# Kernel optimization log

Measured on AMD Instinct MI355X. Metric: run time of the kernel, lower is better.

## Reference

```python
import jax, jax.numpy as jnp
import numpy as np
from jax import lax

IMG_W, IMG_H = 800.0, 320.0
NPTS = 72
N_STRIPS = NPTS - 1
MAX_LANES = 4
NUM_PRIORS = 192
STAGES = 3
B = 512
LIOU_LEN = 15.0
CLS_W, XYT_W, IOU_W, SEG_W = 2.0, 0.2, 2.0, 1.0


def smooth_l1(x):
    ax = jnp.abs(x)
    return jnp.where(ax < 1.0, 0.5 * x * x, ax - 0.5)


def pairwise_line_iou(pred_xs, tgt_xs):
    # pred_xs [P,N] pixel xs, tgt_xs [L,N]; returns [P,L]
    px1, px2 = pred_xs - LIOU_LEN, pred_xs + LIOU_LEN
    tx1, tx2 = tgt_xs - LIOU_LEN, tgt_xs + LIOU_LEN
    ovr = jnp.minimum(px2[:, None, :], tx2[None]) - jnp.maximum(px1[:, None, :], tx1[None])
    union = jnp.maximum(px2[:, None, :], tx2[None]) - jnp.minimum(px1[:, None, :], tx1[None])
    invalid = (tgt_xs < 0) | (tgt_xs >= IMG_W)
    ovr = jnp.where(invalid[None], 0.0, ovr)
    union = jnp.where(invalid[None], 0.0, union)
    return ovr.sum(-1) / (union.sum(-1) + 1e-9)


def focal_sum(logits, target):
    # kornia-style softmax focal loss (alpha=0.25, gamma=2), summed
    p = jax.nn.softmax(logits, axis=1) + 1e-8
    focal = -0.25 * (1.0 - p) ** 2 * jnp.log(p)
    oh = jax.nn.one_hot(target, 2, dtype=logits.dtype)
    return (oh * focal).sum()


def per_sample(pred, tgt):
    # pred [P, 6+N], tgt [L, 6+N]
    L = tgt.shape[0]
    f32 = pred.dtype
    valid = tgt[:, 1] == 1.0
    num_t = valid.sum()
    has_t = num_t > 0

    t_xs = tgt[:, 6:]                          # [L,N] pixel xs (-1e5 = invalid)
    pred_xs_px = pred[:, 6:] * (IMG_W - 1.0)   # [P,N]
    iou_pair = pairwise_line_iou(pred_xs_px, t_xs)  # [P,L] (grad flows for loss)

    # ---------- assignment (stop-grad, mirrors CLRNet dynamic_assign) ----------
    pd = lax.stop_gradient(pred)
    pd_xs = pd[:, 6:] * (IMG_W - 1.0)
    inv_t = (t_xs < 0) | (t_xs >= IMG_W)
    t_len = (~inv_t).sum(1).astype(f32)
    dist = jnp.where(inv_t[None], 0.0, jnp.abs(t_xs[None] - pd_xs[:, None, :])).sum(-1)
    dist = dist / (t_len[None] + 1e-9)         # [P,L]

    def norm_score(x):
        m = jnp.max(jnp.where(valid[None], x, -jnp.inf))
        m = jnp.where(has_t, m, 1.0)
        return 1.0 - x / m + 1e-2

    dist_score = norm_score(dist)
    p_xy = jnp.stack([pd[:, 2] * (IMG_H - 1.0), pd[:, 3] * (IMG_W - 1.0)], 1)
    t_xy = jnp.stack([tgt[:, 2] * (IMG_H - 1.0), tgt[:, 3]], 1)
    sd = jnp.sqrt(((p_xy[:, None] - t_xy[None]) ** 2).sum(-1))
    s_score = norm_score(sd)
    th = jnp.abs(pd[:, 4, None] - tgt[None, :, 4]) * 180.0
    th_score = norm_score(th)
    sp = jax.nn.sigmoid(pd[:, :2])
    neg = -jnp.log(1.0 - sp + 1e-12) * 0.75 * sp ** 2
    pos = -jnp.log(sp + 1e-12) * 0.25 * (1.0 - sp) ** 2
    cls_cost = pos[:, 1] - neg[:, 1]           # all gt labels are 1
    cost = -(dist_score * s_score * th_score) ** 2 * 3.0 + cls_cost[:, None]
    cost = jnp.where(valid[None], cost, jnp.inf)

    # dynamic-k (SimOTA-style)
    iou_sg = jnp.where(valid[None], jnp.maximum(lax.stop_gradient(iou_pair), 0.0), 0.0)
    topk = lax.top_k(iou_sg.T, 4)[0]           # [L,4]
    dyn_k = jnp.maximum(topk.sum(1).astype(jnp.int32), 1)
    ranks = jnp.argsort(jnp.argsort(cost, axis=0), axis=0)
    M = (ranks < dyn_k[None]) & valid[None]
    multi = M.sum(1) > 1
    argmin_col = jnp.argmin(cost, axis=1)
    Mf = M.astype(f32)
    Mf = Mf.at[:, 0].set(jnp.where(multi, 0.0, Mf[:, 0]))
    oh_min = jax.nn.one_hot(argmin_col, L, dtype=f32)
    Mf = jnp.where(multi[:, None] & (oh_min > 0), 1.0, Mf)
    n_match = Mf.sum()

    # ---------- cls loss ----------
    cls_target = (Mf.sum(1) > 0).astype(jnp.int32)
    cls_term = focal_sum(pred[:, :2], cls_target) / jnp.where(has_t, num_t.astype(f32), 1.0)

    # ---------- reg yxtl (smooth L1) ----------
    scale = jnp.array([N_STRIPS, IMG_W - 1.0, 180.0, N_STRIPS], dtype=f32)
    pred_yxtl = pred[:, 2:6] * scale           # [P,4]
    tgt3 = jnp.stack([tgt[:, 2] * N_STRIPS, tgt[:, 3], tgt[:, 4] * 180.0], 1)  # [L,3]
    pred_starts = jnp.clip(jnp.round(lax.stop_gradient(pred[:, 2]) * N_STRIPS), 0, N_STRIPS)
    tgt_starts = jnp.round(tgt[:, 2] * N_STRIPS)
    tgt_len_pair = tgt[None, :, 5] - (pred_starts[:, None] - tgt_starts[None, :])  # [P,L]
    sl = smooth_l1(pred_yxtl[:, None, :3] - tgt3[None]).sum(-1) \
       + smooth_l1(pred_yxtl[:, 3][:, None] - tgt_len_pair)
    reg_term = (Mf * sl).sum() / jnp.maximum(n_match * 4.0, 1.0)
    iou_term = (Mf * (1.0 - iou_pair)).sum() / jnp.maximum(n_match, 1.0)
    zero = jnp.zeros((), f32)
    reg_term = jnp.where(has_t, reg_term, zero)
    iou_term = jnp.where(has_t, iou_term, zero)
    return cls_term, reg_term, iou_term


def setup_inputs() -> dict:
    key = jax.random.key(0)
    ks = jax.random.split(key, 8)
    D = 6 + NPTS
    cls = jax.random.normal(ks[0], (STAGES, B, NUM_PRIORS, 2), jnp.float32)
    rest = jax.random.uniform(ks[1], (STAGES, B, NUM_PRIORS, D - 2), dtype=jnp.float32)
    predictions = jnp.concatenate([cls, rest], -1)

    valid = jax.random.uniform(ks[2], (B, MAX_LANES)) < 0.8
    start = jax.random.randint(ks[3], (B, MAX_LANES), 0, 40)
    length = jax.random.randint(ks[4], (B, MAX_LANES), 10, NPTS)
    end = jnp.minimum(start + length, NPTS)
    idx = jnp.arange(NPTS)
    inside = (idx[None, None] >= start[..., None]) & (idx[None, None] < end[..., None]) & valid[..., None]
    xs = jax.random.uniform(ks[5], (B, MAX_LANES, NPTS), minval=0.0, maxval=IMG_W - 1.0)
    xs = jnp.where(inside, xs, -1e5)
    start_x = jnp.take_along_axis(xs, start[..., None], axis=-1)[..., 0]
    theta = jax.random.uniform(ks[6], (B, MAX_LANES), minval=0.3, maxval=0.9)
    vf = valid.astype(jnp.float32)
    neg = jnp.full((B, MAX_LANES), -1e5, jnp.float32)
    targets = jnp.full((B, MAX_LANES, D), -1e5, jnp.float32)
    targets = targets.at[..., 0].set(1.0 - vf)
    targets = targets.at[..., 1].set(vf)
    targets = targets.at[..., 2].set(jnp.where(valid, start.astype(jnp.float32) / N_STRIPS, neg))
    targets = targets.at[..., 3].set(jnp.where(valid, start_x, neg))
    targets = targets.at[..., 4].set(jnp.where(valid, theta, neg))
    targets = targets.at[..., 5].set(jnp.where(valid, (end - start).astype(jnp.float32), neg))
    targets = targets.at[..., 6:].set(xs)

    seg_loss = jax.random.uniform(ks[7], (), dtype=jnp.float32)
    return {"predictions": predictions, "targets": targets, "seg_loss": seg_loss}


def reference(predictions, targets, seg_loss):
    per_batch = jax.vmap(per_sample)
    cls_l = jnp.zeros((), predictions.dtype)
    reg_l = jnp.zeros((), predictions.dtype)
    iou_l = jnp.zeros((), predictions.dtype)
    for s in range(predictions.shape[0]):  # 3 refine stages (fixed)
        c, r, i = per_batch(predictions[s], targets)
        cls_l = cls_l + c.sum()
        reg_l = reg_l + r.sum()
        iou_l = iou_l + i.sum()
    denom = targets.shape[0] * predictions.shape[0]
    cls_l = cls_l / denom
    reg_l = reg_l / denom
    iou_l = iou_l / denom
    return cls_l * CLS_W + reg_l * XYT_W + iou_l * IOU_W + seg_loss * SEG_W
```

## Files before the change

kernel.cpp:

```cpp
#include <hip/hip_runtime.h>
#include <math.h>

constexpr int kNpts   = 72;
constexpr int kPriors = 192;
constexpr int kLanes  = 4;
constexpr int kBatch  = 512;
constexpr int kStages = 3;
constexpr int kD      = 6 + kNpts;
constexpr int kBlocks = kStages * kBatch;

typedef unsigned long long u64;

__device__ __forceinline__ float smoothL1(float x) {
  float ax = fabsf(x);
  return ax < 1.0f ? 0.5f * x * x : ax - 0.5f;
}

__device__ __forceinline__ unsigned ordF(float f) {
  unsigned b = __float_as_uint(f);
  return (b & 0x80000000u) ? ~b : (b | 0x80000000u);
}

__device__ __forceinline__ void cswapA(u64& a, u64& b) {
  if (b < a) { u64 t = a; a = b; b = t; }
}
__device__ __forceinline__ void cswapD(float& a, float& b) {
  if (b > a) { float t = a; a = b; b = t; }
}
__device__ __forceinline__ u64 umin64(u64 a, u64 b) { return a < b ? a : b; }
__device__ __forceinline__ u64 umax64(u64 a, u64 b) { return a < b ? b : a; }

#define STEP(K, PV) {                                         \
    const float4 t_ = tx4[(K)];                               \
    const float p_ = (PV) * 799.0f;                           \
    ds0 += (t_.x >= 0.0f) ? fabsf(t_.x - p_) : 0.0f;          \
    ds1 += (t_.y >= 0.0f) ? fabsf(t_.y - p_) : 0.0f;          \
    ds2 += (t_.z >= 0.0f) ? fabsf(t_.z - p_) : 0.0f;          \
    ds3 += (t_.w >= 0.0f) ? fabsf(t_.w - p_) : 0.0f; }

#define BATCH18(K0, B)                                            \
    STEP((K0) + 0,  (B##0).x) STEP((K0) + 1,  (B##0).y)           \
    STEP((K0) + 2,  (B##1).x) STEP((K0) + 3,  (B##1).y)           \
    STEP((K0) + 4,  (B##2).x) STEP((K0) + 5,  (B##2).y)           \
    STEP((K0) + 6,  (B##3).x) STEP((K0) + 7,  (B##3).y)           \
    STEP((K0) + 8,  (B##4).x) STEP((K0) + 9,  (B##4).y)           \
    STEP((K0) + 10, (B##5).x) STEP((K0) + 11, (B##5).y)           \
    STEP((K0) + 12, (B##6).x) STEP((K0) + 13, (B##6).y)           \
    STEP((K0) + 14, (B##7).x) STEP((K0) + 15, (B##7).y)           \
    STEP((K0) + 16, (B##8).x) STEP((K0) + 17, (B##8).y)

#define LOADB(B, I0)                                          \
    B##0 = rowv[(I0) + 0]; B##1 = rowv[(I0) + 1];             \
    B##2 = rowv[(I0) + 2]; B##3 = rowv[(I0) + 3];             \
    B##4 = rowv[(I0) + 4]; B##5 = rowv[(I0) + 5];             \
    B##6 = rowv[(I0) + 6]; B##7 = rowv[(I0) + 7];             \
    B##8 = rowv[(I0) + 8];

__global__ __launch_bounds__(192) void clr_loss_kernel(
    const float* __restrict__ pred,
    const float* __restrict__ tgt,
    float* __restrict__ partial) {
  const int blk  = blockIdx.x;
  const int b    = blk & (kBatch - 1);
  const int tid  = threadIdx.x;
  const int wav  = tid >> 6;
  const int lane = tid & 63;

  __shared__ __align__(16) float s_tx[kNpts][kLanes];
  __shared__ float s_hdr[kLanes][6];
  __shared__ float s_cost[kLanes][kPriors];
  __shared__ float s_iou[kLanes][kPriors];
  __shared__ u64   s_k3[kLanes][3];
  __shared__ int   s_dk[kLanes];
  __shared__ float s_sc[3][4];

  const float* tg = tgt + (size_t)b * kLanes * kD;
  for (int t = tid; t < kLanes * kNpts; t += 192) {
    int j = t / kNpts, k = t - j * kNpts;
    s_tx[k][j] = tg[j * kD + 6 + k];
  }
  if (tid < kLanes * 6) {
    int j = tid / 6, c = tid - j * 6;
    s_hdr[j][c] = tg[j * kD + c];
  }
  if (tid >= 64 && tid < 64 + kLanes) {
    int j = tid - 64;
    s_dk[j] = 1; s_k3[j][0] = 0; s_k3[j][1] = 0; s_k3[j][2] = 0;
  }

  const float*  pr   = pred + ((size_t)blk * kPriors + tid) * kD;
  const float2* rowv = (const float2*)pr;
  float2 h0 = rowv[0], h1 = rowv[1], h2 = rowv[2];
  float2 a0, a1, a2, a3, a4, a5, a6, a7, a8;
  float2 b0, b1, b2, b3, b4, b5, b6, b7, b8;
  LOADB(a, 3)
  LOADB(b, 12)
  const float p0 = h0.x, p1 = h0.y, p2 = h1.x, p3 = h1.y, p4 = h2.x, p5 = h2.y;

  __syncthreads();

  bool validL[kLanes];
  int num_t = 0;
#pragma unroll
  for (int j = 0; j < kLanes; ++j) {
    validL[j] = (s_hdr[j][1] == 1.0f);
    num_t += validL[j] ? 1 : 0;
  }
  const bool has_t = num_t > 0;

  float ds0 = 0.0f, ds1 = 0.0f, ds2 = 0.0f, ds3 = 0.0f;
  {
    const float4* tx4 = (const float4*)&s_tx[0][0];
    BATCH18(0, a)
    LOADB(a, 21)
    BATCH18(18, b)
    LOADB(b, 30)
    BATCH18(36, a)
    BATCH18(54, b)
  }
  float ds[kLanes] = {ds0, ds1, ds2, ds3};

  float iou[kLanes], dist[kLanes], sd[kLanes], th[kLanes];
  float md = -INFINITY, ms = -INFINITY, mt = -INFINITY;
  const float py = p2 * 319.0f, pxc = p3 * 799.0f;
#pragma unroll
  for (int j = 0; j < kLanes; ++j) {
    float tlen = validL[j] ? s_hdr[j][5] : 0.0f;
    float ovr = fmaf(tlen, 30.0f, -ds[j]);
    float uni = fmaf(tlen, 30.0f,  ds[j]) + 1e-9f;
    iou[j]  = ovr / uni;
    dist[j] = ds[j] / (tlen + 1e-9f);
    float dy = py - s_hdr[j][2] * 319.0f;
    float dx = pxc - s_hdr[j][3];
    sd[j] = sqrtf(dy * dy + dx * dx);
    th[j] = fabsf(p4 - s_hdr[j][4]) * 180.0f;
    if (validL[j]) {
      md = fmaxf(md, dist[j]);
      ms = fmaxf(ms, sd[j]);
      mt = fmaxf(mt, th[j]);
    }
  }

#pragma unroll
  for (int off = 32; off; off >>= 1) {
    md = fmaxf(md, __shfl_down(md, off, 64));
    ms = fmaxf(ms, __shfl_down(ms, off, 64));
    mt = fmaxf(mt, __shfl_down(mt, off, 64));
  }
  if (lane == 0) { s_sc[wav][0] = md; s_sc[wav][1] = ms; s_sc[wav][2] = mt; }
  __syncthreads();
  md = fmaxf(fmaxf(s_sc[0][0], s_sc[1][0]), s_sc[2][0]);
  ms = fmaxf(fmaxf(s_sc[0][1], s_sc[1][1]), s_sc[2][1]);
  mt = fmaxf(fmaxf(s_sc[0][2], s_sc[1][2]), s_sc[2][2]);
  if (!has_t) { md = 1.0f; ms = 1.0f; mt = 1.0f; }

  const float sp1  = 1.0f / (1.0f + expf(-p1));
  const float neg1 = -logf(1.0f - sp1 + 1e-12f) * 0.75f * sp1 * sp1;
  const float om1  = 1.0f - sp1;
  const float pos1 = -logf(sp1 + 1e-12f) * 0.25f * om1 * om1;
  const float cls_cost = pos1 - neg1;

  float costr[kLanes];
#pragma unroll
  for (int j = 0; j < kLanes; ++j) {
    s_iou[j][tid] = validL[j] ? fmaxf(iou[j], 0.0f) : 0.0f;
    float c;
    if (validL[j]) {
      float a = (1.0f - dist[j] / md) + 0.01f;
      float s = (1.0f - sd[j] / ms) + 0.01f;
      float t = (1.0f - th[j] / mt) + 0.01f;
      float g = a * s * t;
      c = cls_cost - g * g * 3.0f;
    } else {
      c = INFINITY;
    }
    costr[j] = c;
    s_cost[j][tid] = c;
  }
  __syncthreads();

  for (int t = wav; t < 8; t += 3) {
    const int j = t & 3;
    if (!validL[j]) continue;
    if (t < 4) {
      float c0 = s_cost[j][lane], c1 = s_cost[j][lane + 64], c2 = s_cost[j][lane + 128];
      u64 k0 = ((u64)ordF(c0) << 32) | (unsigned)lane;
      u64 k1 = ((u64)ordF(c1) << 32) | (unsigned)(lane + 64);
      u64 k2 = ((u64)ordF(c2) << 32) | (unsigned)(lane + 128);
      cswapA(k0, k1); cswapA(k0, k2); cswapA(k1, k2);
#pragma unroll
      for (int off = 1; off < 64; off <<= 1) {
        u64 b0 = __shfl_xor(k0, off), b1 = __shfl_xor(k1, off), b2 = __shfl_xor(k2, off);
        u64 x0 = umin64(k0, b0), y0 = umax64(k0, b0);
        u64 x1 = umin64(k1, b1);
        u64 mc = umin64(k2, b2);
        k0 = x0;
        k2 = umin64(umax64(y0, x1), mc);
        k1 = umin64(y0, x1);
      }
      if (lane == 0) { s_k3[j][0] = k0; s_k3[j][1] = k1; s_k3[j][2] = k2; }
    } else {
      float t0 = s_iou[j][lane], t1 = s_iou[j][lane + 64], t2 = s_iou[j][lane + 128];
      float t3 = -1.0f;
      cswapD(t0, t1); cswapD(t0, t2); cswapD(t1, t2);
#pragma unroll
      for (int off = 1; off < 64; off <<= 1) {
        float b0 = __shfl_xor(t0, off), b1 = __shfl_xor(t1, off);
        float b2 = __shfl_xor(t2, off), b3 = __shfl_xor(t3, off);
        float m0 = fmaxf(t0, b3), m1 = fmaxf(t1, b2);
        float m2 = fmaxf(t2, b1), m3 = fmaxf(t3, b0);
        cswapD(m0, m2); cswapD(m1, m3); cswapD(m0, m1); cswapD(m2, m3);
        t0 = m0; t1 = m1; t2 = m2; t3 = m3;
      }
      if (lane == 0) {
        float s = ((t0 + t1) + t2) + t3;
        int dk = (int)s;
        if (dk < 1) dk = 1;
        if (dk > 3) dk = 3;
        s_dk[j] = dk;
      }
    }
  }
  __syncthreads();

  int Mi[kLanes];
  int msum = 0;
#pragma unroll
  for (int j = 0; j < kLanes; ++j) {
    u64 myk = ((u64)ordF(costr[j]) << 32) | (unsigned)tid;
    Mi[j] = (validL[j] && myk <= s_k3[j][s_dk[j] - 1]) ? 1 : 0;
    msum += Mi[j];
  }

  float amin = costr[0];
  int aidx = 0;
#pragma unroll
  for (int j = 1; j < kLanes; ++j)
    if (costr[j] < amin) { amin = costr[j]; aidx = j; }

  float Mf[kLanes];
#pragma unroll
  for (int j = 0; j < kLanes; ++j) Mf[j] = (float)Mi[j];
  if (msum > 1) {
    Mf[0] = 0.0f;
    Mf[aidx] = 1.0f;
  }

  const float mfsum = Mf[0] + Mf[1] + Mf[2] + Mf[3];
  const int cls_t = (mfsum > 0.0f) ? 1 : 0;

  const float mx = fmaxf(p0, p1);
  const float e0 = expf(p0 - mx), e1 = expf(p1 - mx);
  const float inv = 1.0f / (e0 + e1);
  const float q = (cls_t ? e1 : e0) * inv + 1e-8f;
  const float omq = 1.0f - q;
  const float focal = -0.25f * omq * omq * logf(q);

  const float pred_start = fminf(fmaxf(rintf(p2 * 71.0f), 0.0f), 71.0f);
  const float py0 = p2 * 71.0f, py1 = p3 * 799.0f, py2t = p4 * 180.0f, py3 = p5 * 71.0f;
  float regc = 0.0f, iouc = 0.0f;
#pragma unroll
  for (int j = 0; j < kLanes; ++j) {
    if (Mf[j] > 0.0f) {
      float t30 = s_hdr[j][2] * 71.0f;
      float t31 = s_hdr[j][3];
      float t32 = s_hdr[j][4] * 180.0f;
      float tstart = rintf(s_hdr[j][2] * 71.0f);
      float tlp = s_hdr[j][5] - (pred_start - tstart);
      regc += smoothL1(py0 - t30) + smoothL1(py1 - t31) + smoothL1(py2t - t32)
            + smoothL1(py3 - tlp);
      iouc += 1.0f - iou[j];
    }
  }

  float v0 = mfsum, v1 = focal, v2 = regc, v3 = iouc;
#pragma unroll
  for (int off = 32; off; off >>= 1) {
    v0 += __shfl_down(v0, off, 64);
    v1 += __shfl_down(v1, off, 64);
    v2 += __shfl_down(v2, off, 64);
    v3 += __shfl_down(v3, off, 64);
  }
  __syncthreads();
  if (lane == 0) {
    s_sc[wav][0] = v0; s_sc[wav][1] = v1; s_sc[wav][2] = v2; s_sc[wav][3] = v3;
  }
  __syncthreads();

  if (tid == 0) {
    float nm      = s_sc[0][0] + s_sc[1][0] + s_sc[2][0];
    float cls_sum = s_sc[0][1] + s_sc[1][1] + s_sc[2][1];
    float reg_sum = s_sc[0][2] + s_sc[1][2] + s_sc[2][2];
    float iou_sum = s_sc[0][3] + s_sc[1][3] + s_sc[2][3];

    float cls_term = cls_sum / (has_t ? (float)num_t : 1.0f);
    float reg_term = has_t ? reg_sum / fmaxf(nm * 4.0f, 1.0f) : 0.0f;
    float iou_term = has_t ? iou_sum / fmaxf(nm, 1.0f) : 0.0f;

    partial[blk] = 2.0f * cls_term + 0.2f * reg_term + 2.0f * iou_term;
  }
}

#undef STEP
#undef BATCH18
#undef LOADB

__global__ __launch_bounds__(256) void clr_reduce(
    const float* __restrict__ partial,
    const float* __restrict__ seg,
    float* __restrict__ out) {
  const int tid  = threadIdx.x;
  const int wav  = tid >> 6;
  const int lane = tid & 63;
  __shared__ float sc[4];

  float s = 0.0f;
#pragma unroll
  for (int i = 0; i < kBlocks / 256; ++i) s += partial[tid + 256 * i];
#pragma unroll
  for (int off = 32; off; off >>= 1) s += __shfl_down(s, off, 64);
  if (lane == 0) sc[wav] = s;
  __syncthreads();
  if (tid == 0) {
    float tot = ((sc[0] + sc[1]) + sc[2]) + sc[3];
    out[0] = tot * (1.0f / (float)kBlocks) + seg[0];
  }
}

extern "C" void kernel_launch(void* const* d_in, const int* in_sizes, int n_in,
                              void* d_out, int out_size, void* d_ws, size_t ws_size,
                              hipStream_t stream) {
  const float* pred = (const float*)d_in[0];
  const float* tgt  = (const float*)d_in[1];
  const float* seg  = (const float*)d_in[2];
  float* out     = (float*)d_out;
  float* partial = (float*)d_ws;

  clr_loss_kernel<<<kBlocks, 192, 0, stream>>>(pred, tgt, partial);
  clr_reduce<<<1, 256, 0, stream>>>(partial, seg, out);
}
```

Measured before the change: 149.0 us.

## Stage prediction tile into LDS with coalesced global_load_lds DMA

Before this change, each thread loaded its own 312-byte prediction row straight from global memory with strided float2 loads. Now the block's whole 192x78 prediction tile is copied into shared memory with 16-byte global_load_lds transfers, where each wave copies contiguous 1 KB chunks, so the global reads are fully coalesced. The per-row distance loop then reads from LDS in a simple unrolled loop instead of juggling two register batches. The cost is about 60 KB of extra LDS per block, which lowers blocks per CU. Row-strided LDS reads may also hit bank conflicts, and the register-level prefetch overlap is lost.

```diff
diff --git a/kernel.cpp b/kernel.cpp
--- a/kernel.cpp
+++ b/kernel.cpp
@@ -8,6 +8,9 @@
 constexpr int kStages = 3;
 constexpr int kD      = 6 + kNpts;
 constexpr int kBlocks = kStages * kBatch;
+constexpr int kTileF  = kPriors * kD;
+constexpr int kTileB  = kTileF * 4;
+constexpr int kChunks = kTileB / 1024;
 
 typedef unsigned long long u64;
 
@@ -29,6 +32,12 @@
 }
 __device__ __forceinline__ u64 umin64(u64 a, u64 b) { return a < b ? a : b; }
 __device__ __forceinline__ u64 umax64(u64 a, u64 b) { return a < b ? b : a; }
+
+__device__ __forceinline__ void gload_lds16(const void* g, void* l) {
+  __builtin_amdgcn_global_load_lds(
+      (const __attribute__((address_space(1))) void*)g,
+      (__attribute__((address_space(3))) void*)l, 16, 0, 0);
+}
 
 #define STEP(K, PV) {                                         \
     const float4 t_ = tx4[(K)];                               \
@@ -37,24 +46,6 @@
     ds1 += (t_.y >= 0.0f) ? fabsf(t_.y - p_) : 0.0f;          \
     ds2 += (t_.z >= 0.0f) ? fabsf(t_.z - p_) : 0.0f;          \
     ds3 += (t_.w >= 0.0f) ? fabsf(t_.w - p_) : 0.0f; }
-
-#define BATCH18(K0, B)                                            \
-    STEP((K0) + 0,  (B##0).x) STEP((K0) + 1,  (B##0).y)           \
-    STEP((K0) + 2,  (B##1).x) STEP((K0) + 3,  (B##1).y)           \
-    STEP((K0) + 4,  (B##2).x) STEP((K0) + 5,  (B##2).y)           \
-    STEP((K0) + 6,  (B##3).x) STEP((K0) + 7,  (B##3).y)           \
-    STEP((K0) + 8,  (B##4).x) STEP((K0) + 9,  (B##4).y)           \
-    STEP((K0) + 10, (B##5).x) STEP((K0) + 11, (B##5).y)           \
-    STEP((K0) + 12, (B##6).x) STEP((K0) + 13, (B##6).y)           \
-    STEP((K0) + 14, (B##7).x) STEP((K0) + 15, (B##7).y)           \
-    STEP((K0) + 16, (B##8).x) STEP((K0) + 17, (B##8).y)
-
-#define LOADB(B, I0)                                          \
-    B##0 = rowv[(I0) + 0]; B##1 = rowv[(I0) + 1];             \
-    B##2 = rowv[(I0) + 2]; B##3 = rowv[(I0) + 3];             \
-    B##4 = rowv[(I0) + 4]; B##5 = rowv[(I0) + 5];             \
-    B##6 = rowv[(I0) + 6]; B##7 = rowv[(I0) + 7];             \
-    B##8 = rowv[(I0) + 8];
 
 __global__ __launch_bounds__(192) void clr_loss_kernel(
     const float* __restrict__ pred,
@@ -66,6 +57,7 @@
   const int wav  = tid >> 6;
   const int lane = tid & 63;
 
+  __shared__ __align__(16) float s_tile[kTileF];
   __shared__ __align__(16) float s_tx[kNpts][kLanes];
   __shared__ float s_hdr[kLanes][6];
   __shared__ float s_cost[kLanes][kPriors];
@@ -74,6 +66,15 @@
   __shared__ int   s_dk[kLanes];
   __shared__ float s_sc[3][4];
 
+  {
+    const char* g0 = (const char*)(pred + (size_t)blk * kTileF);
+    char* l0 = (char*)&s_tile[0];
+    for (int c = wav; c < kChunks; c += 3)
+      gload_lds16(g0 + (c << 10) + (lane << 4), l0 + (c << 10));
+    if (wav == 1 && lane < 32)
+      gload_lds16(g0 + (kChunks << 10) + (lane << 4), l0 + (kChunks << 10));
+  }
+
   const float* tg = tgt + (size_t)b * kLanes * kD;
   for (int t = tid; t < kLanes * kNpts; t += 192) {
     int j = t / kNpts, k = t - j * kNpts;
@@ -88,16 +89,11 @@
     s_dk[j] = 1; s_k3[j][0] = 0; s_k3[j][1] = 0; s_k3[j][2] = 0;
   }
 
-  const float*  pr   = pred + ((size_t)blk * kPriors + tid) * kD;
-  const float2* rowv = (const float2*)pr;
-  float2 h0 = rowv[0], h1 = rowv[1], h2 = rowv[2];
-  float2 a0, a1, a2, a3, a4, a5, a6, a7, a8;
-  float2 b0, b1, b2, b3, b4, b5, b6, b7, b8;
-  LOADB(a, 3)
-  LOADB(b, 12)
+  __syncthreads();
+
+  const float2* rowl = (const float2*)(s_tile + tid * kD);
+  float2 h0 = rowl[0], h1 = rowl[1], h2 = rowl[2];
   const float p0 = h0.x, p1 = h0.y, p2 = h1.x, p3 = h1.y, p4 = h2.x, p5 = h2.y;
-
-  __syncthreads();
 
   bool validL[kLanes];
   int num_t = 0;
@@ -111,12 +107,12 @@
   float ds0 = 0.0f, ds1 = 0.0f, ds2 = 0.0f, ds3 = 0.0f;
   {
     const float4* tx4 = (const float4*)&s_tx[0][0];
-    BATCH18(0, a)
-    LOADB(a, 21)
-    BATCH18(18, b)
-    LOADB(b, 30)
-    BATCH18(36, a)
-    BATCH18(54, b)
+#pragma unroll
+    for (int q = 0; q < 36; ++q) {
+      float2 v = rowl[3 + q];
+      STEP(2 * q,     v.x)
+      STEP(2 * q + 1, v.y)
+    }
   }
   float ds[kLanes] = {ds0, ds1, ds2, ds3};
 
@@ -302,8 +298,6 @@
 }
 
 #undef STEP
-#undef BATCH18
-#undef LOADB
 
 __global__ __launch_bounds__(256) void clr_reduce(
     const float* __restrict__ partial,
```

Result: slower. 161.3 us (+8.3%).
